# Kernel tuning notes

Measured on AMD Instinct MI355X. Metric: run time of the kernel, lower is better.

Reference implementation:

```python
import jax, jax.numpy as jnp
import numpy as np
from jax import lax

SHAPES = [(1024, 1024), (1024, 1024), (512, 512)]  # last matrix is the STORE target
LANE = 8
SIZES = [h * w for h, w in SHAPES]
NUM_EL = sum(SIZES)                    # 2,359,296 labels (all unique -> addr is a permutation)
OFFS = np.cumsum([0] + SIZES)[:-1]
N_ROWS = NUM_EL // LANE                # 294,912 (NUM_EL divisible by lane width)
TH, TW = SHAPES[-1]
N_OPS = TH * TW                        # 262,144 STORE ops


def _conv(x, w, b):
    y = lax.conv_general_dilated(x, w, (1, 1), 'SAME',
                                 dimension_numbers=('NCHW', 'OIHW', 'NCHW'))
    return jax.nn.relu(y + b[None, :, None, None])


def _staged(h, e):
    # h is nonnegative hop distance; staged cache-level multipliers from source
    base = h ** e
    mult = jnp.where(h <= 2., 1.,
           jnp.where(h <= 4., 1.5,
           jnp.where(h <= 8., 2.,
           jnp.where(h <= 16., 3., 5.))))
    return jnp.sum(base * mult)


def reference(mem_logits, conv_w0, conv_b0, conv_w1, conv_b1, conv_w2, conv_b2,
              mem_w, mem_b, proj_w, proj_b):
    # addr[i] = memory address assigned to global label i (torch: addr_map[all_labels[i]] = sort_idx[i])
    addr = jnp.argsort(mem_logits)
    conv_params = [(conv_w0, conv_b0), (conv_w1, conv_b1), (conv_w2, conv_b2)]

    # per-matrix inputs: gather each element's address, run small conv, keep 8-ch features
    feats = []
    for (h, w), off, (cw, cb) in zip(SHAPES, OFFS, conv_params):
        inp = addr[off:off + h * w].astype(jnp.float32).reshape(1, 1, h, w)
        feats.append(_conv(inp, cw, cb).reshape(8, h * w))
    feats_all = jnp.concatenate(feats, axis=1)           # [8, NUM_EL], label order

    # scatter features to their memory addresses (permutation -> no collisions)
    mem = jnp.zeros((8, N_ROWS * LANE), jnp.float32).at[:, addr].set(feats_all)
    mem = mem.reshape(1, 8, N_ROWS, LANE)

    mc = _conv(mem, mem_w, mem_b)                        # [1,16,N_ROWS,LANE]
    # AdaptiveAvgPool2d((4,4)) with divisible dims == exact block means
    pooled = mc.reshape(1, 16, 4, N_ROWS // 4, 4, LANE // 4).mean(axis=(3, 5))
    flat = pooled.reshape(1, -1)                         # [1, 256]
    op_logits = (flat @ proj_w.T + proj_b)[0]            # [N_OPS]

    # address table per op: [src0, src1, dst] (sources tile with i%H, j%W)
    k = jnp.arange(N_OPS)
    i, j = k // TW, k % TW
    cols = [addr[off + (i % h) * w + (j % w)] for (h, w), off in zip(SHAPES[:-1], OFFS[:-1])]
    cols.append(addr[OFFS[-1] + i * TW + j])
    A = jnp.stack(cols, axis=1).astype(jnp.float32)      # [N_OPS, 3]

    order = jnp.argsort(op_logits)
    A = A[order]
    inter = A[1:, 0] - A[:-1, -1]                        # prev dst -> next first src
    intra = (A[:, 1:] - A[:, :-1]).ravel()               # within-op hops
    inter_pen = _staged(jax.nn.relu(inter), 1.) + _staged(jax.nn.relu(-inter), 2.)
    intra_pen = _staged(jax.nn.relu(intra), 1.) + _staged(jax.nn.relu(-intra), 2.)

    return jnp.concatenate([op_logits, jnp.stack([inter_pen, intra_pen])])


def setup_inputs() -> dict:
    key = jax.random.key(0)
    ks = jax.random.split(key, 11)
    n = lambda k, s, sc=1.0: jax.random.normal(k, s, jnp.float32) * sc
    return {
        'mem_logits': n(ks[0], (NUM_EL,)),
        'conv_w0': n(ks[1], (8, 1, 3, 3), 0.1), 'conv_b0': n(ks[2], (8,), 0.1),
        'conv_w1': n(ks[3], (8, 1, 3, 3), 0.1), 'conv_b1': n(ks[4], (8,), 0.1),
        'conv_w2': n(ks[5], (8, 1, 3, 3), 0.1), 'conv_b2': n(ks[6], (8,), 0.1),
        'mem_w': n(ks[7], (16, 8, 3, 3), 0.1), 'mem_b': n(ks[8], (16,), 0.1),
        'proj_w': n(ks[9], (N_OPS, 256), 0.02), 'proj_b': n(ks[10], (N_OPS,), 0.02),
    }
```

## Files before the change

kernel.cpp:

```cpp
#include <hip/hip_runtime.h>
#include <cstdint>
#include <cstddef>

typedef unsigned int u32;
typedef unsigned short u16;
typedef unsigned long long u64;

#define NUM_EL 2359296
#define N_ROWS 294912
#define N_OPS  262144
#define OFF1   1048576
#define OFF2   2097152

#define OFF_F8     18874368ull
#define OFF_COUNTS 56623104ull
#define OFF_POS    56918016ull
#define OFF_PART   57212928ull
#define OFF_FLAT   59572224ull
#define OFF_WT     59573248ull
#define OFF_PPART  59577856ull
#define OFF_OPS    59594240ull
#define OFF_S2     63788544ull

__device__ inline u32 pk_bf16(float a, float b) {
  u32 ua = __float_as_uint(a), ub = __float_as_uint(b);
  ua = (ua + 0x7fffu + ((ua >> 16) & 1u)) >> 16;
  ub = (ub + 0x7fffu + ((ub >> 16) & 1u)) >> 16;
  return ua | (ub << 16);
}

__global__ __launch_bounds__(256) void k_front(const float* __restrict__ x,
                                               u32* __restrict__ keys,
                                               u32* __restrict__ counts0,
                                               const float* __restrict__ mw, float* __restrict__ wt) {
  int b = blockIdx.x, t = threadIdx.x;
  if (b < 288) {
    __shared__ u32 h[256];
    h[t] = 0u;
    __syncthreads();
    int base = b * 8192;
#pragma unroll
    for (int k = 0; k < 32; k++) {
      int i = base + k * 256 + t;
      u32 u = __float_as_uint(x[i]);
      u = (u & 0x80000000u) ? ~u : (u | 0x80000000u);
      keys[i] = u;
      atomicAdd(&h[(u >> 8) & 255u], 1u);
    }
    __syncthreads();
    counts0[t * 288 + b] = h[t];
  } else {
    for (int i = t; i < 1152; i += 256) {
      int oc = i & 15;
      int rest = i >> 4;
      int ic = rest & 7;
      int p = rest >> 3;
      int dr = p / 3, dl = p % 3;
      wt[i] = mw[((oc * 8 + ic) * 3 + dr) * 3 + dl];
    }
  }
}

__global__ __launch_bounds__(512) void k_hist(const u32* __restrict__ keys,
                                              u32* __restrict__ counts, int shift, int nB) {
  __shared__ u32 h[256];
  int t = threadIdx.x;
  if (t < 256) h[t] = 0;
  __syncthreads();
  int base = blockIdx.x * 8192;
#pragma unroll
  for (int k = 0; k < 16; k++) {
    u32 d = (keys[base + t + k * 512] >> shift) & 255u;
    atomicAdd(&h[d], 1u);
  }
  __syncthreads();
  if (t < 256) counts[t * nB + blockIdx.x] = h[t];
}

__global__ __launch_bounds__(256) void k_scan_par(const u32* __restrict__ counts,
                                                  u32* __restrict__ pos, int nB) {
  int d = blockIdx.x, t = threadIdx.x;
  __shared__ u32 red[256];
  u32 s = 0;
  u32 lim = (u32)(d * nB);
  for (u32 i = t; i < lim; i += 256) s += counts[i];
  red[t] = s;
  __syncthreads();
  for (int off = 128; off > 0; off >>= 1) {
    if (t < off) red[t] += red[t + off];
    __syncthreads();
  }
  u32 base = red[0];
  __syncthreads();
  int chunk = (nB + 255) / 256;
  int i0 = t * chunk;
  u32 loc[4];
  u32 lsum = 0;
#pragma unroll 4
  for (int k = 0; k < chunk; k++) {
    int i = i0 + k;
    u32 v = (i < nB) ? counts[d * nB + i] : 0u;
    loc[k] = lsum;
    lsum += v;
  }
  red[t] = lsum;
  __syncthreads();
  for (int off = 1; off < 256; off <<= 1) {
    u32 y = (t >= off) ? red[t - off] : 0u;
    __syncthreads();
    red[t] += y;
    __syncthreads();
  }
  u32 excl = red[t] - lsum;
#pragma unroll 4
  for (int k = 0; k < chunk; k++) {
    int i = i0 + k;
    if (i < nB) pos[d * nB + i] = base + excl + loc[k];
  }
}

__global__ __launch_bounds__(512) void k_scatter(const u32* __restrict__ kin, const u32* __restrict__ vin,
                                                 u32* __restrict__ kout, u32* __restrict__ vout,
                                                 const u32* __restrict__ gbase, int shift, int nB,
                                                 int gen_iota, int mode) {
  __shared__ u32 sk[8192], sv[8192];
  __shared__ u32 whist[8][256];
  __shared__ u32 sbase[256], lstart[256], gdelta[256], red[256];
  int t = threadIdx.x, b = blockIdx.x;
  int base = b * 8192;
  if (t < 256) {
#pragma unroll
    for (int w2 = 0; w2 < 8; w2++) whist[w2][t] = 0;
    sbase[t] = gbase[t * nB + b];
  }
  __syncthreads();
  int w = t >> 6, lane = t & 63;
  u64 lowmask = (1ull << lane) - 1ull;
  u32 kk[16], vv[16], dig[16], rnk[16];
#pragma unroll
  for (int j = 0; j < 16; j++) {
    int idx = base + w * 1024 + j * 64 + lane;
    kk[j] = kin[idx];
    vv[j] = gen_iota ? (u32)idx : vin[idx];
  }
#pragma unroll
  for (int j = 0; j < 16; j++) {
    u32 d = (kk[j] >> shift) & 255u;
    u64 m = ~0ull;
#pragma unroll
    for (int bit = 0; bit < 8; bit++) {
      u64 bal = __ballot((d >> bit) & 1u);
      m &= ((d >> bit) & 1u) ? bal : ~bal;
    }
    u32 rr = (u32)__popcll(m & lowmask);
    u32 cnt = (u32)__popcll(m);
    u32 prev = whist[w][d];
    if (rr == 0) whist[w][d] = prev + cnt;
    dig[j] = d;
    rnk[j] = prev + rr;
  }
  __syncthreads();
  u32 tot = 0;
  if (t < 256) {
    u32 sacc = 0;
#pragma unroll
    for (int ww = 0; ww < 8; ww++) { u32 v = whist[ww][t]; whist[ww][t] = sacc; sacc += v; }
    tot = sacc;
    red[t] = tot;
  }
  __syncthreads();
  for (int off = 1; off < 256; off <<= 1) {
    u32 y = (t < 256 && t >= off) ? red[t - off] : 0u;
    __syncthreads();
    if (t < 256) red[t] += y;
    __syncthreads();
  }
  if (t < 256) {
    u32 lst = red[t] - tot;
    lstart[t] = lst;
    gdelta[t] = sbase[t] - lst;
  }
  __syncthreads();
#pragma unroll
  for (int j = 0; j < 16; j++) {
    u32 d = dig[j];
    u32 lpos = lstart[d] + whist[w][d] + rnk[j];
    sk[lpos] = kk[j];
    sv[lpos] = vv[j];
  }
  __syncthreads();
#pragma unroll
  for (int r = 0; r < 16; r++) {
    int idx = t + r * 512;
    u32 key = sk[idx];
    u32 d = (key >> shift) & 255u;
    u32 gpos = gdelta[d] + (u32)idx;
    u32 val = sv[idx];
    vout[gpos] = val;
    if (mode == 0) kout[gpos] = key;
  }
}

__global__ __launch_bounds__(512) void k_scatter_ops(const u32* __restrict__ kin, const u32* __restrict__ vin,
                                                     const u32* __restrict__ gbase, int shift, int nB,
                                                     const u32* __restrict__ addr, float4* __restrict__ ops) {
  __shared__ u32 sk[8192], sv[8192];
  __shared__ u32 whist[8][256];
  __shared__ u32 sbase[256], lstart[256], gdelta[256], red[256];
  int t = threadIdx.x, b = blockIdx.x;
  int base = b * 8192;
  if (t < 256) {
#pragma unroll
    for (int w2 = 0; w2 < 8; w2++) whist[w2][t] = 0;
    sbase[t] = gbase[t * nB + b];
  }
  __syncthreads();
  int w = t >> 6, lane = t & 63;
  u64 lowmask = (1ull << lane) - 1ull;
  u32 kk[16], vv[16], dig[16], rnk[16];
#pragma unroll
  for (int j = 0; j < 16; j++) {
    int idx = base + w * 1024 + j * 64 + lane;
    kk[j] = kin[idx];
    vv[j] = vin[idx];
  }
#pragma unroll
  for (int j = 0; j < 16; j++) {
    u32 d = (kk[j] >> shift) & 255u;
    u64 m = ~0ull;
#pragma unroll
    for (int bit = 0; bit < 8; bit++) {
      u64 bal = __ballot((d >> bit) & 1u);
      m &= ((d >> bit) & 1u) ? bal : ~bal;
    }
    u32 rr = (u32)__popcll(m & lowmask);
    u32 cnt = (u32)__popcll(m);
    u32 prev = whist[w][d];
    if (rr == 0) whist[w][d] = prev + cnt;
    dig[j] = d;
    rnk[j] = prev + rr;
  }
  __syncthreads();
  u32 tot = 0;
  if (t < 256) {
    u32 sacc = 0;
#pragma unroll
    for (int ww = 0; ww < 8; ww++) { u32 v = whist[ww][t]; whist[ww][t] = sacc; sacc += v; }
    tot = sacc;
    red[t] = tot;
  }
  __syncthreads();
  for (int off = 1; off < 256; off <<= 1) {
    u32 y = (t < 256 && t >= off) ? red[t - off] : 0u;
    __syncthreads();
    if (t < 256) red[t] += y;
    __syncthreads();
  }
  if (t < 256) {
    u32 lst = red[t] - tot;
    lstart[t] = lst;
    gdelta[t] = sbase[t] - lst;
  }
  __syncthreads();
#pragma unroll
  for (int j = 0; j < 16; j++) {
    u32 d = dig[j];
    u32 lpos = lstart[d] + whist[w][d] + rnk[j];
    sk[lpos] = kk[j];
    sv[lpos] = vv[j];
  }
  __syncthreads();
#pragma unroll
  for (int r = 0; r < 16; r++) {
    int idx = t + r * 512;
    u32 key = sk[idx];
    u32 d = (key >> shift) & 255u;
    u32 gpos = gdelta[d] + (u32)idx;
    u32 rv = sv[idx];
    int i = (int)(rv >> 9), jj = (int)(rv & 511);
    float A0 = (float)addr[(i << 10) + jj];
    float A1 = (float)addr[OFF1 + (i << 10) + jj];
    float A2 = (float)addr[OFF2 + (int)rv];
    ops[gpos] = make_float4(A0, A1, A2, 0.0f);
  }
}

__global__ __launch_bounds__(256) void k_conv(const u32* __restrict__ addr,
                                              const float* __restrict__ cw0, const float* __restrict__ cb0,
                                              const float* __restrict__ cw1, const float* __restrict__ cb1,
                                              const float* __restrict__ cw2, const float* __restrict__ cb2,
                                              u16* __restrict__ featsM) {
  int b = blockIdx.x;
  int H, W, lw, off;
  const float *cw, *cb;
  int pix;
  if (b < 4096)      { H = 1024; W = 1024; lw = 10; off = 0;    cw = cw0; cb = cb0; pix = b * 256; }
  else if (b < 8192) { H = 1024; W = 1024; lw = 10; off = OFF1; cw = cw1; cb = cb1; pix = (b - 4096) * 256; }
  else               { H = 512;  W = 512;  lw = 9;  off = OFF2; cw = cw2; cb = cb2; pix = (b - 8192) * 256; }
  pix += threadIdx.x;
  int i = pix >> lw, j = pix & (W - 1);
  u32 m = addr[off + pix];
  float x[3][3];
#pragma unroll
  for (int dr = 0; dr < 3; dr++)
#pragma unroll
    for (int dc = 0; dc < 3; dc++) {
      int r = i + dr - 1, c = j + dc - 1;
      bool inb = ((unsigned)r < (unsigned)H) && ((unsigned)c < (unsigned)W);
      x[dr][dc] = inb ? (float)addr[off + r * W + c] : 0.0f;
    }
  float acc[8];
#pragma unroll
  for (int oc = 0; oc < 8; oc++) {
    float s = cb[oc];
#pragma unroll
    for (int dr = 0; dr < 3; dr++)
#pragma unroll
      for (int dc = 0; dc < 3; dc++)
        s = fmaf(x[dr][dc], cw[oc * 9 + dr * 3 + dc], s);
    acc[oc] = fmaxf(s, 0.0f);
  }
  uint4 pk;
  pk.x = pk_bf16(acc[0], acc[1]);
  pk.y = pk_bf16(acc[2], acc[3]);
  pk.z = pk_bf16(acc[4], acc[5]);
  pk.w = pk_bf16(acc[6], acc[7]);
  *(uint4*)(featsM + (size_t)m * 8) = pk;
}

__global__ __launch_bounds__(256) void k_memconv(const u16* __restrict__ featsM,
                                                 const float* __restrict__ wt,
                                                 const float* __restrict__ mb,
                                                 float* __restrict__ partials) {
  __shared__ float tile[34 * 80];
  __shared__ float pool_s[256 * 17];
  int t = threadIdx.x;
  int r0 = blockIdx.x * 32;
  for (int idx = t; idx < 34 * 8; idx += 256) {
    int rr = idx >> 3, g = idx & 7;
    int r = r0 - 1 + rr;
    float f[8];
    if ((unsigned)r < (unsigned)N_ROWS) {
      uint4 u = *(const uint4*)(featsM + (size_t)(r * 8 + g) * 8);
      f[0] = __uint_as_float(u.x << 16); f[1] = __uint_as_float(u.x & 0xffff0000u);
      f[2] = __uint_as_float(u.y << 16); f[3] = __uint_as_float(u.y & 0xffff0000u);
      f[4] = __uint_as_float(u.z << 16); f[5] = __uint_as_float(u.z & 0xffff0000u);
      f[6] = __uint_as_float(u.w << 16); f[7] = __uint_as_float(u.w & 0xffff0000u);
    } else {
#pragma unroll
      for (int c = 0; c < 8; c++) f[c] = 0.0f;
    }
#pragma unroll
    for (int c = 0; c < 8; c++) tile[rr * 80 + (g + 1) * 8 + c] = f[c];
  }
  for (int idx = t; idx < 34 * 16; idx += 256) {
    int rr = idx >> 4, k = idx & 15;
    int col = (k < 8) ? k : (64 + k);
    tile[rr * 80 + col] = 0.0f;
  }
  __syncthreads();
  int lr = t >> 3, l = t & 7;
  float acc[16];
#pragma unroll
  for (int oc = 0; oc < 16; oc++) acc[oc] = mb[oc];
#pragma unroll
  for (int dr = 0; dr < 3; dr++) {
#pragma unroll
    for (int dl = 0; dl < 3; dl++) {
      const float* src = &tile[(lr + dr) * 80 + (l + dl) * 8];
      float4 a0 = *(const float4*)(src);
      float4 a1 = *(const float4*)(src + 4);
      float xv[8] = {a0.x, a0.y, a0.z, a0.w, a1.x, a1.y, a1.z, a1.w};
      const float* wp = &wt[(dr * 3 + dl) * 128];
#pragma unroll
      for (int ic = 0; ic < 8; ic++) {
#pragma unroll
        for (int oc = 0; oc < 16; oc++)
          acc[oc] = fmaf(xv[ic], wp[ic * 16 + oc], acc[oc]);
      }
    }
  }
#pragma unroll
  for (int oc = 0; oc < 16; oc++) pool_s[t * 17 + oc] = fmaxf(acc[oc], 0.0f);
  __syncthreads();
  if (t < 64) {
    int oc = t >> 2, lb = t & 3;
    float s = 0.0f;
    for (int lr2 = 0; lr2 < 32; lr2++) {
      int t2 = lr2 * 8 + lb * 2;
      s += pool_s[t2 * 17 + oc] + pool_s[(t2 + 1) * 17 + oc];
    }
    partials[(size_t)(oc * 4 + lb) * 9216 + blockIdx.x] = s;
  }
}

__global__ __launch_bounds__(256) void k_pool_final(const float* __restrict__ partials,
                                                    float* __restrict__ flat) {
  int f = blockIdx.x;
  int oc = f >> 4, rb = (f >> 2) & 3, lb = f & 3;
  const float* src = partials + (size_t)(oc * 4 + lb) * 9216 + rb * 2304;
  double s = 0.0;
  for (int i = threadIdx.x; i < 2304; i += 256) s += (double)src[i];
  __shared__ double sd[256];
  sd[threadIdx.x] = s;
  __syncthreads();
  for (int off = 128; off > 0; off >>= 1) {
    if (threadIdx.x < off) sd[threadIdx.x] += sd[threadIdx.x + off];
    __syncthreads();
  }
  if (threadIdx.x == 0) flat[f] = (float)(sd[0] * (1.0 / 147456.0));
}

__global__ __launch_bounds__(256) void k_matvec(const float* __restrict__ pw,
                                                const float* __restrict__ pb,
                                                const float* __restrict__ flat,
                                                float* __restrict__ out,
                                                u32* __restrict__ k2, u32* __restrict__ v2) {
  int t = threadIdx.x;
  int lane = t & 63;
  int g = (blockIdx.x * 256 + t) >> 6;
  float4 f4 = ((const float4*)flat)[lane];
  int row0 = g * 32;
  for (int it = 0; it < 32; it += 2) {
    int row = row0 + it;
    float4 wa = ((const float4*)(pw + (size_t)row * 256))[lane];
    float4 wb = ((const float4*)(pw + (size_t)(row + 1) * 256))[lane];
    float sa = wa.x * f4.x + wa.y * f4.y + wa.z * f4.z + wa.w * f4.w;
    float sb = wb.x * f4.x + wb.y * f4.y + wb.z * f4.z + wb.w * f4.w;
#pragma unroll
    for (int off = 32; off > 0; off >>= 1) {
      sa += __shfl_xor(sa, off, 64);
      sb += __shfl_xor(sb, off, 64);
    }
    if (lane == 0) {
      float ra = sa + pb[row], rb2 = sb + pb[row + 1];
      out[row] = ra;
      out[row + 1] = rb2;
      u32 ua = __float_as_uint(ra), ub = __float_as_uint(rb2);
      ua = (ua & 0x80000000u) ? ~ua : (ua | 0x80000000u);
      ub = (ub & 0x80000000u) ? ~ub : (ub | 0x80000000u);
      k2[row] = ua; k2[row + 1] = ub;
      v2[row] = (u32)row; v2[row + 1] = (u32)(row + 1);
    }
  }
}

__device__ inline double staged_pair(float x) {
  float h = fabsf(x);
  double mult = (h <= 2.f) ? 1.0 : (h <= 4.f) ? 1.5 : (h <= 8.f) ? 2.0 : (h <= 16.f) ? 3.0 : 5.0;
  double hh = (double)h;
  if (x > 0.f) return hh * mult;
  if (x < 0.f) return hh * hh * mult;
  return 0.0;
}

__global__ __launch_bounds__(256) void k_penalty(const float4* __restrict__ ops,
                                                 double* __restrict__ ppart) {
  int k = blockIdx.x * 256 + threadIdx.x;
  float4 a = ops[k];
  double intra = staged_pair(a.y - a.x) + staged_pair(a.z - a.y);
  double inter = 0.0;
  if (k < N_OPS - 1) {
    float4 b = ops[k + 1];
    inter = staged_pair(b.x - a.z);
  }
  __shared__ double s0[256], s1[256];
  s0[threadIdx.x] = inter;
  s1[threadIdx.x] = intra;
  __syncthreads();
  for (int off = 128; off > 0; off >>= 1) {
    if (threadIdx.x < off) {
      s0[threadIdx.x] += s0[threadIdx.x + off];
      s1[threadIdx.x] += s1[threadIdx.x + off];
    }
    __syncthreads();
  }
  if (threadIdx.x == 0) {
    ppart[blockIdx.x] = s0[0];
    ppart[1024 + blockIdx.x] = s1[0];
  }
}

__global__ __launch_bounds__(256) void k_finalize(const double* __restrict__ ppart,
                                                  float* __restrict__ out) {
  int t = threadIdx.x;
  double s0 = 0.0, s1 = 0.0;
  for (int i = t; i < 1024; i += 256) {
    s0 += ppart[i];
    s1 += ppart[1024 + i];
  }
  __shared__ double a0[256], a1[256];
  a0[t] = s0;
  a1[t] = s1;
  __syncthreads();
  for (int off = 128; off > 0; off >>= 1) {
    if (t < off) {
      a0[t] += a0[t + off];
      a1[t] += a1[t + off];
    }
    __syncthreads();
  }
  if (t == 0) {
    out[N_OPS] = (float)a0[0];
    out[N_OPS + 1] = (float)a1[0];
  }
}

extern "C" void kernel_launch(void* const* d_in, const int* in_sizes, int n_in,
                              void* d_out, int out_size, void* d_ws, size_t ws_size,
                              hipStream_t stream) {
  const float* mem_logits = (const float*)d_in[0];
  const float* cw0 = (const float*)d_in[1];
  const float* cb0 = (const float*)d_in[2];
  const float* cw1 = (const float*)d_in[3];
  const float* cb1 = (const float*)d_in[4];
  const float* cw2 = (const float*)d_in[5];
  const float* cb2 = (const float*)d_in[6];
  const float* mw  = (const float*)d_in[7];
  const float* mbb = (const float*)d_in[8];
  const float* pw  = (const float*)d_in[9];
  const float* pb  = (const float*)d_in[10];
  float* out = (float*)d_out;
  char* ws = (char*)d_ws;

  u32* addr      = (u32*)(ws);
  u16* featsM    = (u16*)(ws + OFF_F8);
  u32* kA        = (u32*)(ws + OFF_F8);
  u32* kB        = (u32*)(ws + OFF_F8 + 9437184ull);
  u32* v0        = (u32*)(ws + OFF_F8 + 18874368ull);
  u32* v1        = (u32*)(ws + OFF_F8 + 28311552ull);
  u32* counts    = (u32*)(ws + OFF_COUNTS);
  u32* pos       = (u32*)(ws + OFF_POS);
  float* partials= (float*)(ws + OFF_PART);
  float* flat    = (float*)(ws + OFF_FLAT);
  float* wt      = (float*)(ws + OFF_WT);
  double* ppart  = (double*)(ws + OFF_PPART);
  float4* ops    = (float4*)(ws + OFF_OPS);
  u32* k2A       = (u32*)(ws + OFF_S2);
  u32* k2B       = (u32*)(ws + OFF_S2 + 1048576ull);
  u32* v2A       = (u32*)(ws + OFF_S2 + 2097152ull);
  u32* v2B       = (u32*)(ws + OFF_S2 + 3145728ull);

  k_front<<<289, 256, 0, stream>>>(mem_logits, kA, counts, mw, wt);
  k_scan_par<<<256, 256, 0, stream>>>(counts, pos, 288);
  k_scatter<<<288, 512, 0, stream>>>(kA, nullptr, kB, v0, pos, 8, 288, 1, 0);
  k_hist<<<288, 512, 0, stream>>>(kB, counts, 16, 288);
  k_scan_par<<<256, 256, 0, stream>>>(counts, pos, 288);
  k_scatter<<<288, 512, 0, stream>>>(kB, v0, kA, v1, pos, 16, 288, 0, 0);
  k_hist<<<288, 512, 0, stream>>>(kA, counts, 24, 288);
  k_scan_par<<<256, 256, 0, stream>>>(counts, pos, 288);
  k_scatter<<<288, 512, 0, stream>>>(kA, v1, nullptr, addr, pos, 24, 288, 0, 1);

  k_conv<<<9216, 256, 0, stream>>>(addr, cw0, cb0, cw1, cb1, cw2, cb2, featsM);
  k_memconv<<<9216, 256, 0, stream>>>(featsM, wt, mbb, partials);
  k_pool_final<<<256, 256, 0, stream>>>(partials, flat);

  k_matvec<<<2048, 256, 0, stream>>>(pw, pb, flat, out, k2A, v2A);

  k_hist<<<32, 512, 0, stream>>>(k2A, counts, 8, 32);
  k_scan_par<<<256, 256, 0, stream>>>(counts, pos, 32);
  k_scatter<<<32, 512, 0, stream>>>(k2A, v2A, k2B, v2B, pos, 8, 32, 0, 0);
  k_hist<<<32, 512, 0, stream>>>(k2B, counts, 16, 32);
  k_scan_par<<<256, 256, 0, stream>>>(counts, pos, 32);
  k_scatter<<<32, 512, 0, stream>>>(k2B, v2B, k2A, v2A, pos, 16, 32, 0, 0);
  k_hist<<<32, 512, 0, stream>>>(k2A, counts, 24, 32);
  k_scan_par<<<256, 256, 0, stream>>>(counts, pos, 32);
  k_scatter_ops<<<32, 512, 0, stream>>>(k2A, v2A, pos, 24, 32, addr, ops);

  k_penalty<<<1024, 256, 0, stream>>>(ops, ppart);
  k_finalize<<<1, 256, 0, stream>>>(ppart, out);
}
```

Before: 818.8 us.

## Compute memory conv with bf16 MFMA and keep the feature tile in bf16

The 3x3 memory convolution (8 to 16 channels) is recast as an implicit GEMM that runs on the 16x16x32 bf16 MFMA instruction. Weights are pre-transposed into a padded bf16 layout. The shared tile now holds raw bf16 instead of fp32, and pooling is reduced through wave shuffles and a small shared buffer. The aim is to cut the FMA-bound scalar work and shared-memory traffic in this kernel. The cost is that weights are rounded to bf16, which adds numerical error, and three MFMA steps are issued where only nine of twelve taps are used.

```diff
diff --git a/kernel.cpp b/kernel.cpp
--- a/kernel.cpp
+++ b/kernel.cpp
@@ -5,6 +5,8 @@
 typedef unsigned int u32;
 typedef unsigned short u16;
 typedef unsigned long long u64;
+typedef __attribute__((ext_vector_type(8))) short short8;
+typedef __attribute__((ext_vector_type(4))) float f32x4;
 
 #define NUM_EL 2359296
 #define N_ROWS 294912
@@ -29,10 +31,16 @@
   return ua | (ub << 16);
 }
 
+__device__ inline u16 bf16_1(float a) {
+  u32 ua = __float_as_uint(a);
+  ua = (ua + 0x7fffu + ((ua >> 16) & 1u)) >> 16;
+  return (u16)ua;
+}
+
 __global__ __launch_bounds__(256) void k_front(const float* __restrict__ x,
                                                u32* __restrict__ keys,
                                                u32* __restrict__ counts0,
-                                               const float* __restrict__ mw, float* __restrict__ wt) {
+                                               const float* __restrict__ mw, u16* __restrict__ wtbT) {
   int b = blockIdx.x, t = threadIdx.x;
   if (b < 288) {
     __shared__ u32 h[256];
@@ -50,13 +58,15 @@
     __syncthreads();
     counts0[t * 288 + b] = h[t];
   } else {
-    for (int i = t; i < 1152; i += 256) {
-      int oc = i & 15;
-      int rest = i >> 4;
-      int ic = rest & 7;
-      int p = rest >> 3;
-      int dr = p / 3, dl = p % 3;
-      wt[i] = mw[((oc * 8 + ic) * 3 + dr) * 3 + dl];
+    for (int i = t; i < 1536; i += 256) {
+      int oc = i / 96, k = i % 96;
+      u16 val = 0;
+      if (k < 72) {
+        int tap = k >> 3, ic = k & 7;
+        int dr = tap / 3, dl = tap % 3;
+        val = bf16_1(mw[((oc * 8 + ic) * 3 + dr) * 3 + dl]);
+      }
+      wtbT[i] = val;
     }
   }
 }
@@ -329,68 +339,75 @@
 }
 
 __global__ __launch_bounds__(256) void k_memconv(const u16* __restrict__ featsM,
-                                                 const float* __restrict__ wt,
+                                                 const u16* __restrict__ wtbT,
                                                  const float* __restrict__ mb,
                                                  float* __restrict__ partials) {
-  __shared__ float tile[34 * 80];
-  __shared__ float pool_s[256 * 17];
+  __shared__ u16 tile[34 * 10 * 8];
+  __shared__ float pool4[4][64];
   int t = threadIdx.x;
   int r0 = blockIdx.x * 32;
   for (int idx = t; idx < 34 * 8; idx += 256) {
     int rr = idx >> 3, g = idx & 7;
     int r = r0 - 1 + rr;
-    float f[8];
-    if ((unsigned)r < (unsigned)N_ROWS) {
-      uint4 u = *(const uint4*)(featsM + (size_t)(r * 8 + g) * 8);
-      f[0] = __uint_as_float(u.x << 16); f[1] = __uint_as_float(u.x & 0xffff0000u);
-      f[2] = __uint_as_float(u.y << 16); f[3] = __uint_as_float(u.y & 0xffff0000u);
-      f[4] = __uint_as_float(u.z << 16); f[5] = __uint_as_float(u.z & 0xffff0000u);
-      f[6] = __uint_as_float(u.w << 16); f[7] = __uint_as_float(u.w & 0xffff0000u);
-    } else {
-#pragma unroll
-      for (int c = 0; c < 8; c++) f[c] = 0.0f;
-    }
-#pragma unroll
-    for (int c = 0; c < 8; c++) tile[rr * 80 + (g + 1) * 8 + c] = f[c];
-  }
-  for (int idx = t; idx < 34 * 16; idx += 256) {
-    int rr = idx >> 4, k = idx & 15;
-    int col = (k < 8) ? k : (64 + k);
-    tile[rr * 80 + col] = 0.0f;
-  }
-  __syncthreads();
-  int lr = t >> 3, l = t & 7;
-  float acc[16];
-#pragma unroll
-  for (int oc = 0; oc < 16; oc++) acc[oc] = mb[oc];
-#pragma unroll
-  for (int dr = 0; dr < 3; dr++) {
-#pragma unroll
-    for (int dl = 0; dl < 3; dl++) {
-      const float* src = &tile[(lr + dr) * 80 + (l + dl) * 8];
-      float4 a0 = *(const float4*)(src);
-      float4 a1 = *(const float4*)(src + 4);
-      float xv[8] = {a0.x, a0.y, a0.z, a0.w, a1.x, a1.y, a1.z, a1.w};
-      const float* wp = &wt[(dr * 3 + dl) * 128];
-#pragma unroll
-      for (int ic = 0; ic < 8; ic++) {
-#pragma unroll
-        for (int oc = 0; oc < 16; oc++)
-          acc[oc] = fmaf(xv[ic], wp[ic * 16 + oc], acc[oc]);
-      }
-    }
-  }
-#pragma unroll
-  for (int oc = 0; oc < 16; oc++) pool_s[t * 17 + oc] = fmaxf(acc[oc], 0.0f);
+    uint4 u = make_uint4(0u, 0u, 0u, 0u);
+    if ((unsigned)r < (unsigned)N_ROWS)
+      u = *(const uint4*)(featsM + (size_t)(r * 8 + g) * 8);
+    *(uint4*)(&tile[(rr * 10 + g + 1) * 8]) = u;
+  }
+  for (int idx = t; idx < 34 * 2; idx += 256) {
+    int rr = idx >> 1, side = idx & 1;
+    *(uint4*)(&tile[(rr * 10 + side * 9) * 8]) = make_uint4(0u, 0u, 0u, 0u);
+  }
+  __syncthreads();
+  int w = t >> 6, lane = t & 63;
+  int hi = lane >> 4, lo = lane & 15;
+  short8 bfrag[3];
+#pragma unroll
+  for (int s = 0; s < 3; s++)
+    bfrag[s] = *(const short8*)(wtbT + lo * 96 + s * 32 + hi * 8);
+  int dr_[3], dl_[3];
+  bool valid_[3];
+#pragma unroll
+  for (int s = 0; s < 3; s++) {
+    int tap = s * 4 + hi;
+    valid_[s] = (tap < 9);
+    int tp = valid_[s] ? tap : 0;
+    dr_[s] = tp / 3;
+    dl_[s] = tp % 3;
+  }
+  float bias = mb[lo];
+  int pl = lo & 7;
+  int prow_lo = lo >> 3;
+  float S0 = 0.0f, S1 = 0.0f;
+#pragma unroll
+  for (int tt = 0; tt < 4; tt++) {
+    int prow = w * 8 + tt * 2 + prow_lo;
+    f32x4 acc = {0.0f, 0.0f, 0.0f, 0.0f};
+#pragma unroll
+    for (int s = 0; s < 3; s++) {
+      short8 a = {0, 0, 0, 0, 0, 0, 0, 0};
+      if (valid_[s])
+        a = *(const short8*)(&tile[((prow + dr_[s]) * 10 + pl + dl_[s]) * 8]);
+      acc = __builtin_amdgcn_mfma_f32_16x16x32_bf16(a, bfrag[s], acc, 0, 0, 0);
+    }
+    float v0 = fmaxf(acc[0] + bias, 0.0f);
+    float v1 = fmaxf(acc[1] + bias, 0.0f);
+    float v2 = fmaxf(acc[2] + bias, 0.0f);
+    float v3 = fmaxf(acc[3] + bias, 0.0f);
+    S0 += v0 + v1;
+    S1 += v2 + v3;
+  }
+  S0 += __shfl_xor(S0, 32, 64);
+  S1 += __shfl_xor(S1, 32, 64);
+  if (hi < 2) {
+    int lb0 = (hi & 1) * 2;
+    pool4[w][lo * 4 + lb0]     = S0;
+    pool4[w][lo * 4 + lb0 + 1] = S1;
+  }
   __syncthreads();
   if (t < 64) {
-    int oc = t >> 2, lb = t & 3;
-    float s = 0.0f;
-    for (int lr2 = 0; lr2 < 32; lr2++) {
-      int t2 = lr2 * 8 + lb * 2;
-      s += pool_s[t2 * 17 + oc] + pool_s[(t2 + 1) * 17 + oc];
-    }
-    partials[(size_t)(oc * 4 + lb) * 9216 + blockIdx.x] = s;
+    float s = pool4[0][t] + pool4[1][t] + pool4[2][t] + pool4[3][t];
+    partials[(size_t)t * 9216 + blockIdx.x] = s;
   }
 }
 
@@ -533,7 +550,7 @@
   u32* pos       = (u32*)(ws + OFF_POS);
   float* partials= (float*)(ws + OFF_PART);
   float* flat    = (float*)(ws + OFF_FLAT);
-  float* wt      = (float*)(ws + OFF_WT);
+  u16* wtbT      = (u16*)(ws + OFF_WT);
   double* ppart  = (double*)(ws + OFF_PPART);
   float4* ops    = (float4*)(ws + OFF_OPS);
   u32* k2A       = (u32*)(ws + OFF_S2);
@@ -541,7 +558,7 @@
   u32* v2A       = (u32*)(ws + OFF_S2 + 2097152ull);
   u32* v2B       = (u32*)(ws + OFF_S2 + 3145728ull);
 
-  k_front<<<289, 256, 0, stream>>>(mem_logits, kA, counts, mw, wt);
+  k_front<<<289, 256, 0, stream>>>(mem_logits, kA, counts, mw, wtbT);
   k_scan_par<<<256, 256, 0, stream>>>(counts, pos, 288);
   k_scatter<<<288, 512, 0, stream>>>(kA, nullptr, kB, v0, pos, 8, 288, 1, 0);
   k_hist<<<288, 512, 0, stream>>>(kB, counts, 16, 288);
@@ -552,7 +569,7 @@
   k_scatter<<<288, 512, 0, stream>>>(kA, v1, nullptr, addr, pos, 24, 288, 0, 1);
 
   k_conv<<<9216, 256, 0, stream>>>(addr, cw0, cb0, cw1, cb1, cw2, cb2, featsM);
-  k_memconv<<<9216, 256, 0, stream>>>(featsM, wt, mbb, partials);
+  k_memconv<<<9216, 256, 0, stream>>>(featsM, wtbT, mbb, partials);
   k_pool_final<<<256, 256, 0, stream>>>(partials, flat);
 
   k_matvec<<<2048, 256, 0, stream>>>(pw, pb, flat, out, k2A, v2A);
```

Measured after the change: 752.1 us. 8.1% less time.
